# Performance work log

Measured on AMD Instinct MI355X. Metric: run time of the kernel, lower is better.

The kernel has to match this reference:

```python
import math
import jax, jax.numpy as jnp
import numpy as np

B, T, D, H = 4, 2048, 1024, 16
HD = D // H


def setup_inputs() -> dict:
    key = jax.random.key(0)
    ks = jax.random.split(key, 5)
    s = 1.0 / math.sqrt(D)  # linear-layer-ish init scale
    x = jax.random.normal(ks[0], (B, T, D), dtype=jnp.float32)
    wq = jax.random.normal(ks[1], (D, D), dtype=jnp.float32) * s
    wk = jax.random.normal(ks[2], (D, D), dtype=jnp.float32) * s
    wv = jax.random.normal(ks[3], (D, D), dtype=jnp.float32) * s
    wo = jax.random.normal(ks[4], (D, D), dtype=jnp.float32) * s
    bq = jnp.zeros((D,), jnp.float32)
    bk = jnp.zeros((D,), jnp.float32)
    bv = jnp.zeros((D,), jnp.float32)
    bo = jnp.zeros((D,), jnp.float32)
    # causal 0/1 mask, broadcast over batch and heads: [1, 1, T, T]
    mask = jnp.tril(jnp.ones((T, T), jnp.int32))[None, None]
    return {"x": x, "wq": wq, "bq": bq, "wk": wk, "bk": bk,
            "wv": wv, "bv": bv, "wo": wo, "bo": bo, "mask": mask}


def reference(x, wq, bq, wk, bk, wv, bv, wo, bo, mask):
    b, t, d = x.shape
    # separate QKV linears (x_cond defaults to x -> self-attention)
    q = x @ wq.T + bq
    k = x @ wk.T + bk
    v = x @ wv.T + bv
    # [b, t, h, hd] -> [b, h, t, hd]
    q = q.reshape(b, t, H, HD).transpose(0, 2, 1, 3)
    k = k.reshape(b, t, H, HD).transpose(0, 2, 1, 3)
    v = v.reshape(b, t, H, HD).transpose(0, 2, 1, 3)
    scale = 1.0 / math.sqrt(HD)
    attn = jnp.einsum('bhtd,bhsd->bhts', q, k) * scale  # [b, h, t, t]
    attn = jnp.where(mask[:, :, :t, :t] == 0, jnp.float32(-jnp.inf), attn)
    attn = jax.nn.softmax(attn, axis=-1)
    # dropout is identity in eval mode
    out = jnp.einsum('bhts,bhsd->bhtd', attn, v)  # [b, h, t, hd]
    out = out.transpose(0, 2, 1, 3).reshape(b, t, d)
    return out @ wo.T + bo
```

## Files before the change

### kernel.cpp

```cpp
#include <hip/hip_runtime.h>
#include <cstdint>

typedef __bf16 bf16x8 __attribute__((ext_vector_type(8)));
typedef float f32x4 __attribute__((ext_vector_type(4)));
typedef uint32_t u32x4 __attribute__((ext_vector_type(4)));
typedef unsigned short u16;

#define B_ 4
#define T_ 2048
#define D_ 1024
#define H_ 16
#define HD_ 64
#define M_ (B_*T_)
#define QSCALE 0.1803368801111204f

__device__ __forceinline__ u16 f2bf(float f) {
  union { float f; uint32_t u; } x; x.f = f;
  uint32_t u = x.u;
  uint32_t r = (u + 0x7FFFu + ((u >> 16) & 1u)) >> 16;
  return (u16)r;
}

__device__ __forceinline__ uint32_t pkbf(float a, float b) {
  union { float f; uint32_t u; } x, y; x.f = a; y.f = b;
  uint32_t t0 = x.u + 0x8000u, t1 = y.u + 0x8000u;
  return __builtin_amdgcn_perm(t1, t0, 0x07060302u);
}

__device__ __forceinline__ bf16x8 ld8(const u16* p) {
  return *(const bf16x8*)p;
}

__device__ __forceinline__ void gl_lds16(const u16* g, u16* l) {
  __builtin_amdgcn_global_load_lds(
      (__attribute__((address_space(1))) void*)(g),
      (__attribute__((address_space(3))) void*)(l), 16, 0, 0);
}

__global__ void cvt_all(const float* __restrict__ x, const float* __restrict__ wq,
                        const float* __restrict__ wk, const float* __restrict__ wv,
                        const float* __restrict__ wo,
                        u16* __restrict__ xb, u16* __restrict__ wqb, u16* __restrict__ wkb,
                        u16* __restrict__ wvb, u16* __restrict__ wob) {
  const long NX = (long)M_ * D_;
  long i = ((long)blockIdx.x * 256 + threadIdx.x) * 4;
  const float* s; u16* d; long j;
  if (i < NX) { s = x; d = xb; j = i; }
  else {
    long r = i - NX; int seg = (int)(r >> 20); j = r & ((1 << 20) - 1);
    s = seg == 0 ? wq : seg == 1 ? wk : seg == 2 ? wv : wo;
    d = seg == 0 ? wqb : seg == 1 ? wkb : seg == 2 ? wvb : wob;
  }
  float4 v = *(const float4*)(s + j);
  ushort4 o;
  o.x = f2bf(v.x); o.y = f2bf(v.y); o.z = f2bf(v.z); o.w = f2bf(v.w);
  *(ushort4*)(d + j) = o;
}


template <int PH>
__device__ __forceinline__ void ldA_ph(bf16x8 (&af)[2][2], const u16* buf,
                                       int wr, int lanem, int quad) {
#pragma unroll
  for (int mi = 0; mi < 2; ++mi)
#pragma unroll
    for (int ks = 0; ks < 2; ++ks) {
      int row = wr * 64 + (PH * 2 + mi) * 16 + lanem;
      int off = row * 64 + ((ks * 32 + quad * 8) ^ ((lanem & 7) << 3));
      af[mi][ks] = ld8(buf + off);
    }
}

__device__ __forceinline__ void ldB_all(bf16x8 (&bfr)[4][2], const u16* buf,
                                        int wc, int lanem, int quad) {
#pragma unroll
  for (int nj = 0; nj < 4; ++nj)
#pragma unroll
    for (int ks = 0; ks < 2; ++ks) {
      int row = 256 + wc * 64 + nj * 16 + lanem;
      int off = row * 64 + ((ks * 32 + quad * 8) ^ ((lanem & 7) << 3));
      bfr[nj][ks] = ld8(buf + off);
    }
}

template <int PH>
__device__ __forceinline__ void mfmaPH(f32x4 (&acc)[4][4], const bf16x8 (&af)[2][2],
                                       const bf16x8 (&bfr)[4][2]) {
#pragma unroll
  for (int mi = 0; mi < 2; ++mi)
#pragma unroll
    for (int nj = 0; nj < 4; ++nj)
#pragma unroll
      for (int ks = 0; ks < 2; ++ks)
        acc[PH * 2 + mi][nj] = __builtin_amdgcn_mfma_f32_16x16x32_bf16(
            af[mi][ks], bfr[nj][ks], acc[PH * 2 + mi][nj], 0, 0, 0);
}

#define PH_PRE()                                        \
  __builtin_amdgcn_s_barrier();                         \
  asm volatile("s_waitcnt lgkmcnt(0)" ::: "memory");    \
  __builtin_amdgcn_sched_barrier(0);                    \
  __builtin_amdgcn_s_setprio(1)

#define PH_POST()                                       \
  __builtin_amdgcn_s_setprio(0);                        \
  __builtin_amdgcn_s_barrier()

#define GEMM_V3_KLOOP(Asrc, Bsrc)                                              \
  u16* p0 = &sm.S[0][0][0];                                                    \
  u16* p1 = &sm.S[1][0][0];                                                    \
  u16* p2 = &sm.S[2][0][0];                                                    \
  auto stage = [&](u16* bufbase, int u, int k0) {                              \
    const u16* src = (u < 4)                                                   \
        ? Asrc + (size_t)(m0 + u * 64 + wv * 8 + grow) * D_ + k0 + gcol        \
        : Bsrc + (size_t)(n0 + (u - 4) * 64 + wv * 8 + grow) * D_ + k0 + gcol; \
    gl_lds16(src, bufbase + (u * 64 + wv * 8) * 64);                           \
  };                                                                           \
  _Pragma("unroll")                                                            \
  for (int u = 0; u < 6; ++u) stage(p0, u, 0);                                 \
  _Pragma("unroll")                                                            \
  for (int u = 0; u < 6; ++u) stage(p1, u, 64);                                \
  asm volatile("s_waitcnt vmcnt(6)" ::: "memory");                             \
  __builtin_amdgcn_s_barrier();                                                \
  for (int kt = 0; kt < 16; ++kt) {                                            \
    const int k2 = (kt + 2) << 6;                                              \
    ldA_ph<0>(af, p0, wr, lanem, quad);                                        \
    ldB_all(bfr, p0, wc, lanem, quad);                                         \
    if (kt < 14) { stage(p2, 0, k2); stage(p2, 1, k2); stage(p2, 2, k2); }     \
    PH_PRE();                                                                  \
    mfmaPH<0>(acc, af, bfr);                                                   \
    PH_POST();                                                                 \
    ldA_ph<1>(af, p0, wr, lanem, quad);                                        \
    if (kt < 14) { stage(p2, 3, k2); stage(p2, 4, k2); stage(p2, 5, k2); }     \
    __builtin_amdgcn_s_barrier();                                              \
    asm volatile("s_waitcnt lgkmcnt(0)" ::: "memory");                         \
    __builtin_amdgcn_sched_barrier(0);                                         \
    __builtin_amdgcn_s_setprio(1);                                             \
    mfmaPH<1>(acc, af, bfr);                                                   \
    __builtin_amdgcn_s_setprio(0);                                             \
    if (kt < 14)       asm volatile("s_waitcnt vmcnt(6)" ::: "memory");        \
    else if (kt == 14) asm volatile("s_waitcnt vmcnt(0)" ::: "memory");        \
    __builtin_amdgcn_s_barrier();                                              \
    u16* t = p0; p0 = p1; p1 = p2; p2 = t;                                     \
  }

__global__ __launch_bounds__(512, 2)
void gemm_qkv(const u16* __restrict__ A, const u16* __restrict__ Bw,
              const float* __restrict__ bq, const float* __restrict__ bk,
              const float* __restrict__ bv,
              u16* __restrict__ qb, u16* __restrict__ kb, u16* __restrict__ vtb) {
  __shared__ union {
    u16 S[3][384][64];
    u16 C[256 * 136];
  } sm;

  const int tid = threadIdx.x;
  const int wv = tid >> 6, lane = tid & 63;
  const int lanem = lane & 15, quad = lane >> 4;
  const int wr = wv >> 1, wc = wv & 1;

  const int l = ((int)blockIdx.x & 7) * 96 + ((int)blockIdx.x >> 3);
  const int n0 = (l % 24) * 128, m0 = (l / 24) * 256;

  const int grow = lane >> 3;
  const int gcol = (((lane & 7) ^ grow) * 8);

  f32x4 acc[4][4];
#pragma unroll
  for (int a = 0; a < 4; ++a)
#pragma unroll
    for (int b = 0; b < 4; ++b) acc[a][b] = (f32x4){0.f, 0.f, 0.f, 0.f};

  bf16x8 af[2][2];
  bf16x8 bfr[4][2];

  GEMM_V3_KLOOP(A, Bw);

  const int seg = n0 >> 10, n0l = n0 & 1023;
  const int bb = m0 >> 11, tl0 = m0 & (T_ - 1);

  if (seg == 2) {
    __syncthreads();
#pragma unroll
    for (int a = 0; a < 4; ++a)
#pragma unroll
      for (int nj = 0; nj < 4; ++nj) {
        int ncol = wc * 64 + nj * 16 + lanem;
        float bvv = bv[n0l + ncol];
        int mb = wr * 64 + a * 16 + quad * 4;
        ushort4 w4;
        w4.x = f2bf(acc[a][nj][0] + bvv);
        w4.y = f2bf(acc[a][nj][1] + bvv);
        w4.z = f2bf(acc[a][nj][2] + bvv);
        w4.w = f2bf(acc[a][nj][3] + bvv);
        *(ushort4*)&sm.C[ncol * 264 + mb] = w4;
      }
    __syncthreads();
#pragma unroll
    for (int it = 0; it < 8; ++it) {
      int chunk = it * 512 + tid;
      int nrow = chunk >> 5, c8 = chunk & 31;
      int gnl = n0l + nrow;
      int hh = gnl >> 6, hd = gnl & 63;
      *(uint4*)&vtb[(((size_t)bb * H_ + hh) * HD_ + hd) * T_ + tl0 + c8 * 8] =
          *(const uint4*)&sm.C[nrow * 264 + c8 * 8];
    }
  } else {
    const float* bias = seg == 0 ? bq : bk;
    u16* out = seg == 0 ? qb : kb;
    const float sc = seg == 0 ? QSCALE : 1.0f;
    __syncthreads();
#pragma unroll
    for (int a = 0; a < 4; ++a)
#pragma unroll
      for (int nj = 0; nj < 4; ++nj) {
        int col = wc * 64 + nj * 16 + lanem;
        float bvv = bias[n0l + col];
        int r = wr * 64 + a * 16 + quad * 4;
#pragma unroll
        for (int i = 0; i < 4; ++i)
          sm.C[(r + i) * 136 + col] = f2bf((acc[a][nj][i] + bvv) * sc);
      }
    __syncthreads();
#pragma unroll
    for (int it = 0; it < 8; ++it) {
      int chunk = it * 512 + tid;
      int row = chunk >> 4, c8 = chunk & 15;
      int col0 = c8 * 8;
      int hh = (n0l + col0) >> 6, hd = col0 & 63;
      int t = tl0 + row;
      *(uint4*)&out[(((size_t)bb * H_ + hh) * T_ + t) * HD_ + hd] =
          *(const uint4*)&sm.C[row * 136 + col0];
    }
  }
}

__global__ __launch_bounds__(512, 2)
void gemm_wo(const u16* __restrict__ A, const u16* __restrict__ Bw,
             const float* __restrict__ bias, float* __restrict__ Co) {
  __shared__ union {
    u16 S[3][384][64];
    u16 C[256 * 136];
  } sm;

  const int tid = threadIdx.x;
  const int wv = tid >> 6, lane = tid & 63;
  const int lanem = lane & 15, quad = lane >> 4;
  const int wr = wv >> 1, wc = wv & 1;

  const int l = ((int)blockIdx.x & 7) * 32 + ((int)blockIdx.x >> 3);
  const int n0 = (l & 7) * 128, m0 = (l >> 3) * 256;

  const int grow = lane >> 3;
  const int gcol = (((lane & 7) ^ grow) * 8);

  f32x4 acc[4][4];
#pragma unroll
  for (int a = 0; a < 4; ++a)
#pragma unroll
    for (int b = 0; b < 4; ++b) acc[a][b] = (f32x4){0.f, 0.f, 0.f, 0.f};

  bf16x8 af[2][2];
  bf16x8 bfr[4][2];

  GEMM_V3_KLOOP(A, Bw);

#pragma unroll
  for (int nj = 0; nj < 4; ++nj) {
    int gn = n0 + wc * 64 + nj * 16 + lanem;
    float bvv = bias[gn];
#pragma unroll
    for (int a = 0; a < 4; ++a)
#pragma unroll
      for (int i = 0; i < 4; ++i) {
        int gm = m0 + wr * 64 + a * 16 + quad * 4 + i;
        Co[(size_t)gm * D_ + gn] = acc[a][nj][i] + bvv;
      }
  }
}

__global__ __launch_bounds__(256, 4)
void flash4(const u16* __restrict__ qb, const u16* __restrict__ kb,
            const u16* __restrict__ vtb, u16* __restrict__ ob) {
  __shared__ u16 Ks[2][2][64][32];
  __shared__ u16 Vs[2][2][64][32];
  int tid = threadIdx.x, wv = tid >> 6, lane = tid & 63;
  int lanem = lane & 15, quad = lane >> 4;
  int h = blockIdx.y, b = blockIdx.z;
  int z = (int)blockIdx.z;
  int qt = ((int)blockIdx.x ^ ((z & 1) * 15) ^ ((z >> 1) * 3)) & 15;
  size_t bh = (size_t)b * H_ + h;
  int qrow0 = qt * 128 + wv * 32;
  const u16* Qg = qb + (bh * T_ + qrow0) * HD_;
  const u16* Kg = kb + bh * T_ * HD_;
  const u16* Vg = vtb + bh * HD_ * T_;

  int slot = tid >> 2, r = slot & 15;
  int key = (slot >> 5) * 32 + (r >> 2) * 8 + ((slot >> 4) & 1) * 4 + (r & 3);
  const u16* gK = Kg + (size_t)key * HD_ + (tid & 3) * 8;
  const u16* gV = Vg + (size_t)slot * T_ + (tid & 3) * 8;

  bf16x8 bq[2][2];
#pragma unroll
  for (int mi = 0; mi < 2; ++mi)
#pragma unroll
    for (int ks = 0; ks < 2; ++ks)
      bq[mi][ks] = ld8(&Qg[(size_t)(mi * 16 + lanem) * HD_ + ks * 32 + quad * 8]);

  f32x4 acc_o[2][4];
  float lsum[2][4];
#pragma unroll
  for (int mi = 0; mi < 2; ++mi) {
#pragma unroll
    for (int c = 0; c < 4; ++c) lsum[mi][c] = 0.f;
#pragma unroll
    for (int ni = 0; ni < 4; ++ni) acc_o[mi][ni] = (f32x4){0.f, 0.f, 0.f, 0.f};
  }

  int nIter = qt * 2 + 2;
  int myTiles = (qrow0 >> 6) + 1;

#define STAGE_KV(bufi, s0c)                                                 \
  do {                                                                      \
    gl_lds16(gK + (size_t)(s0c) * HD_,      &Ks[bufi][0][0][0] + wv * 512); \
    gl_lds16(gK + (size_t)(s0c) * HD_ + 32, &Ks[bufi][1][0][0] + wv * 512); \
    gl_lds16(gV + (s0c),                    &Vs[bufi][0][0][0] + wv * 512); \
    gl_lds16(gV + (s0c) + 32,               &Vs[bufi][1][0][0] + wv * 512); \
  } while (0)

  STAGE_KV(0, 0);
  for (int it = 0; it < nIter; ++it) {
    __builtin_amdgcn_s_waitcnt(0);
    __syncthreads();
    if (it + 1 < nIter) STAGE_KV((it + 1) & 1, (it + 1) * 64);
    if (it >= myTiles) continue;
    int s0 = it * 64, buf = it & 1;

    f32x4 accs[2][4];
#pragma unroll
    for (int mi = 0; mi < 2; ++mi)
#pragma unroll
      for (int ni = 0; ni < 4; ++ni) accs[mi][ni] = (f32x4){0.f, 0.f, 0.f, 0.f};
#pragma unroll
    for (int ks = 0; ks < 2; ++ks)
#pragma unroll
      for (int ni = 0; ni < 4; ++ni) {
        bf16x8 kf = ld8(&Ks[buf][ks][ni * 16 + lanem][quad * 8]);
        accs[0][ni] = __builtin_amdgcn_mfma_f32_16x16x32_bf16(kf, bq[0][ks], accs[0][ni], 0, 0, 0);
        accs[1][ni] = __builtin_amdgcn_mfma_f32_16x16x32_bf16(kf, bq[1][ks], accs[1][ni], 0, 0, 0);
      }

    if (s0 + 63 > qrow0) {
#pragma unroll
      for (int mi = 0; mi < 2; ++mi) {
        int qg = qrow0 + mi * 16 + lanem;
#pragma unroll
        for (int ni = 0; ni < 4; ++ni)
#pragma unroll
          for (int i = 0; i < 4; ++i) {
            int sl = (ni >> 1) * 32 + quad * 8 + (ni & 1) * 4 + i;
            float p = (s0 + sl > qg) ? 0.f : __builtin_amdgcn_exp2f(accs[mi][ni][i]);
            accs[mi][ni][i] = p;
            lsum[mi][i] += p;
          }
      }
    } else {
#pragma unroll
      for (int mi = 0; mi < 2; ++mi)
#pragma unroll
        for (int ni = 0; ni < 4; ++ni)
#pragma unroll
          for (int i = 0; i < 4; ++i) {
            float p = __builtin_amdgcn_exp2f(accs[mi][ni][i]);
            accs[mi][ni][i] = p;
            lsum[mi][i] += p;
          }
    }

#pragma unroll
    for (int c = 0; c < 2; ++c) {
      u32x4 pk0, pk1;
      pk0[0] = pkbf(accs[0][c * 2][0], accs[0][c * 2][1]);
      pk0[1] = pkbf(accs[0][c * 2][2], accs[0][c * 2][3]);
      pk0[2] = pkbf(accs[0][c * 2 + 1][0], accs[0][c * 2 + 1][1]);
      pk0[3] = pkbf(accs[0][c * 2 + 1][2], accs[0][c * 2 + 1][3]);
      pk1[0] = pkbf(accs[1][c * 2][0], accs[1][c * 2][1]);
      pk1[1] = pkbf(accs[1][c * 2][2], accs[1][c * 2][3]);
      pk1[2] = pkbf(accs[1][c * 2 + 1][0], accs[1][c * 2 + 1][1]);
      pk1[3] = pkbf(accs[1][c * 2 + 1][2], accs[1][c * 2 + 1][3]);
      bf16x8 bp0 = __builtin_bit_cast(bf16x8, pk0);
      bf16x8 bp1 = __builtin_bit_cast(bf16x8, pk1);
#pragma unroll
      for (int ni = 0; ni < 4; ++ni) {
        bf16x8 vf = ld8(&Vs[buf][c][ni * 16 + lanem][quad * 8]);
        acc_o[0][ni] = __builtin_amdgcn_mfma_f32_16x16x32_bf16(vf, bp0, acc_o[0][ni], 0, 0, 0);
        acc_o[1][ni] = __builtin_amdgcn_mfma_f32_16x16x32_bf16(vf, bp1, acc_o[1][ni], 0, 0, 0);
      }
    }
  }
#undef STAGE_KV

#pragma unroll
  for (int mi = 0; mi < 2; ++mi) {
    float v = (lsum[mi][0] + lsum[mi][1]) + (lsum[mi][2] + lsum[mi][3]);
    v += __shfl_xor(v, 16);
    v += __shfl_xor(v, 32);
    float inv = 1.f / v;
    int q = qrow0 + mi * 16 + lanem;
    u16* og = ob + ((size_t)b * T_ + q) * D_ + h * HD_;
#pragma unroll
    for (int ni = 0; ni < 4; ++ni) {
      ushort4 st;
      st.x = f2bf(acc_o[mi][ni][0] * inv);
      st.y = f2bf(acc_o[mi][ni][1] * inv);
      st.z = f2bf(acc_o[mi][ni][2] * inv);
      st.w = f2bf(acc_o[mi][ni][3] * inv);
      *(ushort4*)(og + ni * 16 + quad * 4) = st;
    }
  }
}

extern "C" void kernel_launch(void* const* d_in, const int* in_sizes, int n_in,
                              void* d_out, int out_size, void* d_ws, size_t ws_size,
                              hipStream_t stream) {
  const float* x  = (const float*)d_in[0];
  const float* wq = (const float*)d_in[1];
  const float* bq = (const float*)d_in[2];
  const float* wk = (const float*)d_in[3];
  const float* bk = (const float*)d_in[4];
  const float* wv = (const float*)d_in[5];
  const float* bv = (const float*)d_in[6];
  const float* wo = (const float*)d_in[7];
  const float* bo = (const float*)d_in[8];

  char* ws = (char*)d_ws;
  const size_t MB = 1ull << 20;
  u16* xb   = (u16*)(ws + 0 * MB);
  u16* wqkv = (u16*)(ws + 16 * MB);
  u16* wob  = (u16*)(ws + 22 * MB);
  u16* qb   = (u16*)(ws + 24 * MB);
  u16* kb   = (u16*)(ws + 40 * MB);
  u16* vtb  = (u16*)(ws + 56 * MB);
  u16* ob   = (u16*)(ws + 72 * MB);

  cvt_all<<<(M_ * D_ + 4 * D_ * D_) / 1024, 256, 0, stream>>>(
      x, wq, wk, wv, wo, xb, wqkv, wqkv + (size_t)D_ * D_, wqkv + 2 * (size_t)D_ * D_, wob);

  gemm_qkv<<<768, 512, 0, stream>>>(xb, wqkv, bq, bk, bv, qb, kb, vtb);

  flash4<<<dim3(T_ / 128, H_, B_), 256, 0, stream>>>(qb, kb, vtb, ob);

  gemm_wo<<<256, 512, 0, stream>>>(ob, wob, bo, (float*)d_out);
}
```

Measured before the change: 257.9 us.

## Collapse two-phase GEMM k-loop into single phase and add MFMA priority hints

The QKV and output GEMM k-loops drop their two-phase ping-pong schedule, which split A-fragment loads, global staging and MFMAs into halves separated by extra barriers. Each iteration now loads all A and B fragments at once, issues all six staging loads, and runs every MFMA in one block. This removes two workgroup barriers per k-step, but raises A-fragment register use and changes how LDS reads, global loads and MFMAs overlap. Separately, the flash attention kernel wraps its QK and PV MFMA sections in s_setprio to favour matrix issue over other waves.

```diff
diff --git a/kernel.cpp b/kernel.cpp
--- a/kernel.cpp
+++ b/kernel.cpp
@@ -58,14 +58,13 @@
 }
 
 
-template <int PH>
-__device__ __forceinline__ void ldA_ph(bf16x8 (&af)[2][2], const u16* buf,
-                                       int wr, int lanem, int quad) {
-#pragma unroll
-  for (int mi = 0; mi < 2; ++mi)
+__device__ __forceinline__ void ldA_all(bf16x8 (&af)[4][2], const u16* buf,
+                                        int wr, int lanem, int quad) {
+#pragma unroll
+  for (int mi = 0; mi < 4; ++mi)
 #pragma unroll
     for (int ks = 0; ks < 2; ++ks) {
-      int row = wr * 64 + (PH * 2 + mi) * 16 + lanem;
+      int row = wr * 64 + mi * 16 + lanem;
       int off = row * 64 + ((ks * 32 + quad * 8) ^ ((lanem & 7) << 3));
       af[mi][ks] = ld8(buf + off);
     }
@@ -83,30 +82,19 @@
     }
 }
 
-template <int PH>
-__device__ __forceinline__ void mfmaPH(f32x4 (&acc)[4][4], const bf16x8 (&af)[2][2],
-                                       const bf16x8 (&bfr)[4][2]) {
-#pragma unroll
-  for (int mi = 0; mi < 2; ++mi)
+__device__ __forceinline__ void mfmaAll(f32x4 (&acc)[4][4], const bf16x8 (&af)[4][2],
+                                        const bf16x8 (&bfr)[4][2]) {
+#pragma unroll
+  for (int mi = 0; mi < 4; ++mi)
 #pragma unroll
     for (int nj = 0; nj < 4; ++nj)
 #pragma unroll
       for (int ks = 0; ks < 2; ++ks)
-        acc[PH * 2 + mi][nj] = __builtin_amdgcn_mfma_f32_16x16x32_bf16(
-            af[mi][ks], bfr[nj][ks], acc[PH * 2 + mi][nj], 0, 0, 0);
-}
-
-#define PH_PRE()                                        \
-  __builtin_amdgcn_s_barrier();                         \
-  asm volatile("s_waitcnt lgkmcnt(0)" ::: "memory");    \
-  __builtin_amdgcn_sched_barrier(0);                    \
-  __builtin_amdgcn_s_setprio(1)
-
-#define PH_POST()                                       \
-  __builtin_amdgcn_s_setprio(0);                        \
-  __builtin_amdgcn_s_barrier()
-
-#define GEMM_V3_KLOOP(Asrc, Bsrc)                                              \
+        acc[mi][nj] = __builtin_amdgcn_mfma_f32_16x16x32_bf16(
+            af[mi][ks], bfr[nj][ks], acc[mi][nj], 0, 0, 0);
+}
+
+#define GEMM_V5_KLOOP(Asrc, Bsrc)                                              \
   u16* p0 = &sm.S[0][0][0];                                                    \
   u16* p1 = &sm.S[1][0][0];                                                    \
   u16* p2 = &sm.S[2][0][0];                                                    \
@@ -124,20 +112,18 @@
   __builtin_amdgcn_s_barrier();                                                \
   for (int kt = 0; kt < 16; ++kt) {                                            \
     const int k2 = (kt + 2) << 6;                                              \
-    ldA_ph<0>(af, p0, wr, lanem, quad);                                        \
+    ldA_all(af, p0, wr, lanem, quad);                                          \
     ldB_all(bfr, p0, wc, lanem, quad);                                         \
-    if (kt < 14) { stage(p2, 0, k2); stage(p2, 1, k2); stage(p2, 2, k2); }     \
-    PH_PRE();                                                                  \
-    mfmaPH<0>(acc, af, bfr);                                                   \
-    PH_POST();                                                                 \
-    ldA_ph<1>(af, p0, wr, lanem, quad);                                        \
-    if (kt < 14) { stage(p2, 3, k2); stage(p2, 4, k2); stage(p2, 5, k2); }     \
-    __builtin_amdgcn_s_barrier();                                              \
+    if (kt < 14) {                                                             \
+      stage(p2, 0, k2); stage(p2, 1, k2); stage(p2, 2, k2);                    \
+      stage(p2, 3, k2); stage(p2, 4, k2); stage(p2, 5, k2);                    \
+    }                                                                          \
     asm volatile("s_waitcnt lgkmcnt(0)" ::: "memory");                         \
     __builtin_amdgcn_sched_barrier(0);                                         \
     __builtin_amdgcn_s_setprio(1);                                             \
-    mfmaPH<1>(acc, af, bfr);                                                   \
+    mfmaAll(acc, af, bfr);                                                     \
     __builtin_amdgcn_s_setprio(0);                                             \
+    __builtin_amdgcn_sched_barrier(0);                                         \
     if (kt < 14)       asm volatile("s_waitcnt vmcnt(6)" ::: "memory");        \
     else if (kt == 14) asm volatile("s_waitcnt vmcnt(0)" ::: "memory");        \
     __builtin_amdgcn_s_barrier();                                              \
@@ -171,10 +157,10 @@
 #pragma unroll
     for (int b = 0; b < 4; ++b) acc[a][b] = (f32x4){0.f, 0.f, 0.f, 0.f};
 
-  bf16x8 af[2][2];
+  bf16x8 af[4][2];
   bf16x8 bfr[4][2];
 
-  GEMM_V3_KLOOP(A, Bw);
+  GEMM_V5_KLOOP(A, Bw);
 
   const int seg = n0 >> 10, n0l = n0 & 1023;
   const int bb = m0 >> 11, tl0 = m0 & (T_ - 1);
@@ -260,10 +246,10 @@
 #pragma unroll
     for (int b = 0; b < 4; ++b) acc[a][b] = (f32x4){0.f, 0.f, 0.f, 0.f};
 
-  bf16x8 af[2][2];
+  bf16x8 af[4][2];
   bf16x8 bfr[4][2];
 
-  GEMM_V3_KLOOP(A, Bw);
+  GEMM_V5_KLOOP(A, Bw);
 
 #pragma unroll
   for (int nj = 0; nj < 4; ++nj) {
@@ -341,6 +327,7 @@
     for (int mi = 0; mi < 2; ++mi)
 #pragma unroll
       for (int ni = 0; ni < 4; ++ni) accs[mi][ni] = (f32x4){0.f, 0.f, 0.f, 0.f};
+    __builtin_amdgcn_s_setprio(1);
 #pragma unroll
     for (int ks = 0; ks < 2; ++ks)
 #pragma unroll
@@ -349,6 +336,7 @@
         accs[0][ni] = __builtin_amdgcn_mfma_f32_16x16x32_bf16(kf, bq[0][ks], accs[0][ni], 0, 0, 0);
         accs[1][ni] = __builtin_amdgcn_mfma_f32_16x16x32_bf16(kf, bq[1][ks], accs[1][ni], 0, 0, 0);
       }
+    __builtin_amdgcn_s_setprio(0);
 
     if (s0 + 63 > qrow0) {
 #pragma unroll
@@ -390,12 +378,14 @@
       pk1[3] = pkbf(accs[1][c * 2 + 1][2], accs[1][c * 2 + 1][3]);
       bf16x8 bp0 = __builtin_bit_cast(bf16x8, pk0);
       bf16x8 bp1 = __builtin_bit_cast(bf16x8, pk1);
+      __builtin_amdgcn_s_setprio(1);
 #pragma unroll
       for (int ni = 0; ni < 4; ++ni) {
         bf16x8 vf = ld8(&Vs[buf][c][ni * 16 + lanem][quad * 8]);
         acc_o[0][ni] = __builtin_amdgcn_mfma_f32_16x16x32_bf16(vf, bp0, acc_o[0][ni], 0, 0, 0);
         acc_o[1][ni] = __builtin_amdgcn_mfma_f32_16x16x32_bf16(vf, bp1, acc_o[1][ni], 0, 0, 0);
       }
+      __builtin_amdgcn_s_setprio(0);
     }
   }
 #undef STAGE_KV
```

Result: no change. 257.8 us, median of 2 (-0.1%).
